# Kernel tuning notes

Hardware: AMD Instinct MI355X
Metric: run time of the kernel (lower is better)

The kernel has to match this reference:

```python
import jax, jax.numpy as jnp
import numpy as np

IMG = 1024.0            # image H = W
PRE_NMS, POST_NMS = 2000, 1000
NMS_THR, MIN_SZ = 0.7, 16.0
B = 16                  # batch of images


def _make_anchors():
    # Standard FPN anchor tiling: strides {4..64}, one scale per level, 3 ratios.
    strides = [4, 8, 16, 32, 64]
    scales = [32.0, 64.0, 128.0, 256.0, 512.0]
    ratios = [0.5, 1.0, 2.0]
    out = []
    for s, sc in zip(strides, scales):
        n = int(IMG) // s
        c = (np.arange(n, dtype=np.float32) + 0.5) * s
        xs, ys = np.meshgrid(c, c, indexing="xy")
        ctr = np.stack([xs.ravel(), ys.ravel()], -1)              # (n*n, 2) cx,cy
        wh = np.array([[sc * np.sqrt(1.0 / r), sc * np.sqrt(r)] for r in ratios],
                      dtype=np.float32)                           # (3, 2)
        b = np.concatenate([ctr[:, None, :] - wh[None] / 2,
                            ctr[:, None, :] + wh[None] / 2], -1)  # (n*n, 3, 4)
        out.append(b.reshape(-1, 4))
    return np.concatenate(out, 0).astype(np.float32)              # (261888, 4)


def setup_inputs() -> dict:
    key = jax.random.key(0)
    k1, k2 = jax.random.split(key)
    anchors = jnp.asarray(_make_anchors())
    A = anchors.shape[0]
    deltas = jax.random.normal(k1, (B, A, 4), dtype=jnp.float32) * 0.1
    scores = jax.random.uniform(k2, (B, A), dtype=jnp.float32)    # post-sigmoid objectness
    return {"anchors": anchors, "deltas": deltas, "scores": scores}


def _decode(anchors, deltas):
    # decode_boxes: deltas (tx,ty,tw,th) applied to anchors; dw/dh clamped at 4.0
    aw = anchors[:, 2] - anchors[:, 0]
    ah = anchors[:, 3] - anchors[:, 1]
    ax = anchors[:, 0] + 0.5 * aw
    ay = anchors[:, 1] + 0.5 * ah
    dx, dy = deltas[..., 0], deltas[..., 1]
    dw = jnp.minimum(deltas[..., 2], 4.0)
    dh = jnp.minimum(deltas[..., 3], 4.0)
    px = dx * aw + ax
    py = dy * ah + ay
    pw = jnp.exp(dw) * aw
    ph = jnp.exp(dh) * ah
    return jnp.stack([px - 0.5 * pw, py - 0.5 * ph,
                      px + 0.5 * pw, py + 0.5 * ph], -1)


def _box_iou(a, b):
    area_a = (a[:, 2] - a[:, 0]) * (a[:, 3] - a[:, 1])
    area_b = (b[:, 2] - b[:, 0]) * (b[:, 3] - b[:, 1])
    lt = jnp.maximum(a[:, None, :2], b[None, :, :2])
    rb = jnp.minimum(a[:, None, 2:], b[None, :, 2:])
    wh = jnp.clip(rb - lt, 0.0)
    inter = wh[..., 0] * wh[..., 1]
    return inter / (area_a[:, None] + area_b[None, :] - inter + 1e-6)


def _filter_one(props, s):
    # RegionProposalNetwork._filter: clip -> size filter -> topk(pre_nms) -> NMS -> post_nms
    x1 = jnp.clip(props[:, 0], 0.0, IMG)
    y1 = jnp.clip(props[:, 1], 0.0, IMG)
    x2 = jnp.clip(props[:, 2], 0.0, IMG)
    y2 = jnp.clip(props[:, 3], 0.0, IMG)
    valid = (x2 - x1 >= MIN_SZ) & (y2 - y1 >= MIN_SZ)
    ms = jnp.where(valid, s, -jnp.inf)                 # mask instead of boolean gather (jit)
    vals, idx = jax.lax.top_k(ms, PRE_NMS)            # sorted desc, as in scores.topk
    b = jnp.stack([x1, y1, x2, y2], -1)[idx]          # (PRE_NMS, 4)
    iou = _box_iou(b, b)                              # (PRE_NMS, PRE_NMS)
    later = jnp.arange(PRE_NMS)

    def body(i, keep):
        # suppress later boxes overlapping a still-kept box i (greedy NMS)
        sup = (iou[i] > NMS_THR) & keep[i] & (later > i)
        return keep & ~sup

    keep = jax.lax.fori_loop(0, PRE_NMS, body, jnp.ones(PRE_NMS, dtype=bool))
    fs = jnp.where(keep, vals, -jnp.inf)
    fv, fi = jax.lax.top_k(fs, POST_NMS)              # kept boxes, desc score order
    good = jnp.isfinite(fv)                           # padding mask for suppressed slots
    boxes = jnp.where(good[:, None], b[fi], 0.0)
    sc = jnp.where(good, fv, 0.0)
    return jnp.concatenate([boxes, sc[:, None]], -1)  # (POST_NMS, 5) = (x1,y1,x2,y2,score)


def reference(anchors, deltas, scores):
    props = _decode(anchors, deltas)                  # (B, A, 4)
    return jax.vmap(_filter_one)(props, scores)       # (B, POST_NMS, 5)
```

## Files before the change

kernel.cpp:

```cpp
#include <hip/hip_runtime.h>
#include <stdint.h>
#include <math.h>


#define IMGF 1024.0f
#define PRE_NMS 2000
#define POST_NMS 1000
#define NMS_THR 0.7f
#define MIN_SZ 16.0f
#define CAP 4096
#define SEL 2048
#define NW (SEL / 64)
#define CNT_STRIDE 32
#define KEY_NEGINF 0x007FFFFFu
#define MAXCHUNK 12

__device__ __forceinline__ uint32_t f2key(float f) {
  uint32_t u = __float_as_uint(f);
  return (u & 0x80000000u) ? ~u : (u | 0x80000000u);
}
__device__ __forceinline__ float key2f(uint32_t k) {
  uint32_t u = (k & 0x80000000u) ? (k & 0x7FFFFFFFu) : ~k;
  return __uint_as_float(u);
}

__device__ __forceinline__ unsigned long long readlane_u64(unsigned long long v,
                                                           int lane) {
  unsigned int lo = __builtin_amdgcn_readlane((unsigned int)v, lane);
  unsigned int hi = __builtin_amdgcn_readlane((unsigned int)(v >> 32), lane);
  return ((unsigned long long)hi << 32) | lo;
}

__device__ __forceinline__ float4 decode_clip(float4 anc, float4 dlt) {
  float aw = anc.z - anc.x;
  float ah = anc.w - anc.y;
  float ax = anc.x + 0.5f * aw;
  float ay = anc.y + 0.5f * ah;
  float dw = fminf(dlt.z, 4.0f);
  float dh = fminf(dlt.w, 4.0f);
  float px = dlt.x * aw + ax;
  float py = dlt.y * ah + ay;
  float pw = expf(dw) * aw;
  float ph = expf(dh) * ah;
  float x1 = px - 0.5f * pw, y1 = py - 0.5f * ph;
  float x2 = px + 0.5f * pw, y2 = py + 0.5f * ph;
  x1 = fminf(fmaxf(x1, 0.0f), IMGF);
  y1 = fminf(fmaxf(y1, 0.0f), IMGF);
  x2 = fminf(fmaxf(x2, 0.0f), IMGF);
  y2 = fminf(fmaxf(y2, 0.0f), IMGF);
  return make_float4(x1, y1, x2, y2);
}

__global__ void k_decode(const float4* __restrict__ anchors,
                         const float4* __restrict__ deltas,
                         const float* __restrict__ scores,
                         uint32_t* __restrict__ keys,
                         uint32_t* __restrict__ chist,
                         int A, int chunks) {
  int b = blockIdx.y;
  int t = threadIdx.x;
  int lane = t & 63;
  __shared__ uint32_t shist[256];
  shist[t] = 0;
  __syncthreads();
  int base_a = blockIdx.x * (chunks * 256);
  for (int c = 0; c < chunks; c++) {
    int a = base_a + c * 256 + t;
    bool inb = a < A;
    int ac = inb ? a : (A - 1);
    size_t i = (size_t)b * A + ac;
    float4 box = decode_clip(anchors[ac], deltas[i]);
    bool valid = (box.z - box.x >= MIN_SZ) && (box.w - box.y >= MIN_SZ);
    float ms = valid ? scores[i] : -INFINITY;
    uint32_t k = f2key(ms);
    if (inb) keys[i] = k;
    uint32_t bucket = k >> 24;
    bool fin = inb && (k != KEY_NEGINF);
    unsigned long long match = __ballot(fin);
#pragma unroll
    for (int bit = 0; bit < 8; bit++) {
      bool hb = (bucket >> bit) & 1;
      unsigned long long bb = __ballot(hb && fin);
      match &= hb ? bb : ~bb;
    }
    if (fin && (__ffsll((long long)match) - 1 == lane))
      atomicAdd(&shist[bucket], (uint32_t)__popcll(match));
  }
  __syncthreads();
  uint32_t v = shist[t];
  if (v) atomicAdd(&chist[b * 256 + t], v);
}

__global__ void k_coarse(const uint32_t* __restrict__ chist,
                         int* __restrict__ cbArr,
                         uint32_t* __restrict__ cumArr) {
  int b = blockIdx.x;
  int t = threadIdx.x;
  __shared__ uint32_t sA[256];
  sA[t] = chist[b * 256 + t];
  for (int d = 1; d < 256; d <<= 1) {
    __syncthreads();
    uint32_t v = sA[t] + ((t + d < 256) ? sA[t + d] : 0u);
    __syncthreads();
    sA[t] = v;
  }
  __syncthreads();
  if (t == 0 && sA[0] < PRE_NMS) {
    cbArr[b] = -1;
    cumArr[b] = 0;
  }
  uint32_t nxt = (t < 255) ? sA[t + 1] : 0u;
  if (sA[t] >= PRE_NMS && nxt < PRE_NMS) {
    cbArr[b] = t;
    cumArr[b] = nxt;
  }
}

__global__ void k_fine(const uint32_t* __restrict__ keys,
                       const int* __restrict__ cbArr,
                       uint32_t* __restrict__ fhist,
                       int A, int chunks) {
  int b = blockIdx.y;
  int t = threadIdx.x;
  int cb = cbArr[b];
  if (cb < 0) return;
  __shared__ uint32_t shist[256];
  shist[t] = 0;
  __syncthreads();
  int base_a = blockIdx.x * (chunks * 256);
  uint32_t cbu = (uint32_t)cb;
  for (int c = 0; c < chunks; c++) {
    int a = base_a + c * 256 + t;
    if (a >= A) break;
    uint32_t k = keys[(size_t)b * A + a];
    if ((k >> 24) == cbu && k != KEY_NEGINF)
      atomicAdd(&shist[(k >> 16) & 0xFFu], 1u);
  }
  __syncthreads();
  uint32_t v = shist[t];
  if (v) atomicAdd(&fhist[b * 256 + t], v);
}

__global__ void k_thresh(const uint32_t* __restrict__ fhist,
                         const int* __restrict__ cbArr,
                         const uint32_t* __restrict__ cumArr,
                         uint32_t* __restrict__ thresh,
                         uint32_t* __restrict__ cnts) {
  int b = blockIdx.x;
  int t = threadIdx.x;
  __shared__ uint32_t sA[256];
  if (t < 2) cnts[b * CNT_STRIDE + t] = 0;
  int cb = cbArr[b];
  if (cb < 0) {
    if (t == 0) thresh[b] = 0u;
    return;
  }
  uint32_t cumAbove = cumArr[b];
  sA[t] = fhist[b * 256 + t];
  for (int d = 1; d < 256; d <<= 1) {
    __syncthreads();
    uint32_t v = sA[t] + ((t + d < 256) ? sA[t + d] : 0u);
    __syncthreads();
    sA[t] = v;
  }
  __syncthreads();
  uint32_t nxt = (t < 255) ? sA[t + 1] : 0u;
  if (cumAbove + sA[t] >= PRE_NMS && cumAbove + nxt < PRE_NMS)
    thresh[b] = (uint32_t)((cb << 8) | t);
}

__global__ void k_gather(const uint32_t* __restrict__ keys,
                         const uint32_t* __restrict__ thresh,
                         uint32_t* __restrict__ cnts,
                         unsigned long long* __restrict__ cand_sort,
                         float4* __restrict__ sel_box,
                         float* __restrict__ sel_score,
                         int A, int chunks) {
  int b = blockIdx.y;
  int t = threadIdx.x;
  int lane = t & 63;
  int w = t >> 6;
  if (blockIdx.x < SEL / 256) {
    int r = blockIdx.x * 256 + t;
    sel_score[(size_t)b * SEL + r] = -INFINITY;
    sel_box[(size_t)b * SEL + r] = make_float4(0.0f, 0.0f, 0.0f, 0.0f);
  }
  __shared__ unsigned long long s_mA[MAXCHUNK * 4], s_mT[MAXCHUNK * 4];
  __shared__ uint32_t s_offA[MAXCHUNK * 4], s_offT[MAXCHUNK * 4];
  __shared__ uint32_t s_cA[MAXCHUNK * 4], s_cT[MAXCHUNK * 4];
  __shared__ uint32_t s_baseA, s_baseT;
  uint32_t beta = thresh[b];
  uint32_t kreg[MAXCHUNK];
  int base_a = blockIdx.x * (chunks * 256);
  for (int c = 0; c < chunks; c++) {
    int a = base_a + c * 256 + t;
    bool inb = a < A;
    uint32_t k = inb ? keys[(size_t)b * A + a] : KEY_NEGINF;
    kreg[c] = k;
    uint32_t bk = k >> 16;
    bool fin = (k != KEY_NEGINF);
    unsigned long long mA = __ballot(fin && (bk > beta));
    unsigned long long mT = __ballot(fin && (bk == beta));
    if (lane == 0) {
      s_mA[c * 4 + w] = mA;
      s_mT[c * 4 + w] = mT;
    }
  }
  __syncthreads();
  if (t < chunks * 4) {
    s_cA[t] = (uint32_t)__popcll(s_mA[t]);
    s_cT[t] = (uint32_t)__popcll(s_mT[t]);
  }
  __syncthreads();
  if (t == 0) {
    uint32_t accA = 0, accT = 0;
    for (int id = 0; id < chunks * 4; id++) {
      s_offA[id] = accA;
      accA += s_cA[id];
      s_offT[id] = accT;
      accT += s_cT[id];
    }
    s_baseA = accA ? atomicAdd(&cnts[b * CNT_STRIDE + 0], accA) : 0u;
    s_baseT = accT ? atomicAdd(&cnts[b * CNT_STRIDE + 1], accT) : 0u;
  }
  __syncthreads();
  uint32_t baseA = s_baseA, baseT = s_baseT;
  unsigned long long lower = ((unsigned long long)1 << lane) - 1;
  for (int c = 0; c < chunks; c++) {
    int id = c * 4 + w;
    unsigned long long mA = s_mA[id], mT = s_mT[id];
    bool above = (mA >> lane) & 1;
    bool tie = (mT >> lane) & 1;
    if (!(above || tie)) continue;
    int pos;
    if (above) {
      pos = (int)(baseA + s_offA[id] + (uint32_t)__popcll(mA & lower));
      if (pos >= PRE_NMS) continue;
    } else {
      pos = CAP - 1 - (int)(baseT + s_offT[id] + (uint32_t)__popcll(mT & lower));
      if (pos < PRE_NMS) continue;
    }
    int a = base_a + c * 256 + t;
    cand_sort[(size_t)b * CAP + pos] =
        ((unsigned long long)kreg[c] << 32) | (uint32_t)(~(uint32_t)a);
  }
}

__global__ void k_rank(const unsigned long long* __restrict__ cand_sort,
                       const uint32_t* __restrict__ cnts,
                       const float4* __restrict__ anchors,
                       const float4* __restrict__ deltas,
                       float4* __restrict__ sel_box,
                       float* __restrict__ sel_score, int A) {
  int b = blockIdx.y;
  int t = threadIdx.x;
  uint32_t c1 = cnts[b * CNT_STRIDE + 0];
  if (c1 > PRE_NMS) c1 = PRE_NMS;
  uint32_t c2 = cnts[b * CNT_STRIDE + 1];
  if (c2 > CAP - PRE_NMS) c2 = CAP - PRE_NMS;
  int loTie = CAP - (int)c2;
  int bs = blockIdx.x * 256;
  if (bs >= (int)c1 && bs + 256 <= loTie) return;
  int s = bs + t;
  bool live = (s < (int)c1) || (s >= loTie);
  unsigned long long myKey = live ? cand_sort[(size_t)b * CAP + s] : 0ull;
  __shared__ unsigned long long tile[256];
  int rank = 0;
  for (int ts = 0; ts < CAP; ts += 256) {
    if (ts >= (int)c1 && ts + 256 <= loTie) continue;
    int idx = ts + t;
    bool lv = (idx < (int)c1) || (idx >= loTie);
    __syncthreads();
    tile[t] = lv ? cand_sort[(size_t)b * CAP + idx] : 0ull;
    __syncthreads();
    if (live) {
#pragma unroll 8
      for (int j = 0; j < 256; j++) rank += (tile[j] > myKey) ? 1 : 0;
    }
  }
  if (live && rank < SEL) {
    uint32_t a = ~((uint32_t)myKey);
    float4 box = decode_clip(anchors[a], deltas[(size_t)b * A + a]);
    sel_score[(size_t)b * SEL + rank] = key2f((uint32_t)(myKey >> 32));
    sel_box[(size_t)b * SEL + rank] = box;
  }
}

__global__ void __launch_bounds__(64)
k_nmsmask(const float4* __restrict__ sel_box,
          unsigned long long* __restrict__ mask,
          unsigned long long* __restrict__ maskT) {
  int jb = blockIdx.x;
  int rp = blockIdx.y;
  int ib0 = rp * 4;
  if (jb < ib0) return;
  int b = blockIdx.z;
  int t = threadIdx.x;
  __shared__ float4 colb[64];
  colb[t] = sel_box[(size_t)b * SEL + jb * 64 + t];
  float4 a0 = sel_box[(size_t)b * SEL + (ib0 + 0) * 64 + t];
  float4 a1 = sel_box[(size_t)b * SEL + (ib0 + 1) * 64 + t];
  float4 a2 = sel_box[(size_t)b * SEL + (ib0 + 2) * 64 + t];
  float4 a3 = sel_box[(size_t)b * SEL + (ib0 + 3) * 64 + t];
  float ar0 = (a0.z - a0.x) * (a0.w - a0.y);
  float ar1 = (a1.z - a1.x) * (a1.w - a1.y);
  float ar2 = (a2.z - a2.x) * (a2.w - a2.y);
  float ar3 = (a3.z - a3.x) * (a3.w - a3.y);
  unsigned long long b0 = 0ull, b1 = 0ull, b2 = 0ull, b3 = 0ull;
#pragma unroll 2
  for (int jj = 0; jj < 64; jj++) {
    float4 bb = colb[jj];
    float area_b = (bb.z - bb.x) * (bb.w - bb.y);
    {
      float ltx = fmaxf(a0.x, bb.x), lty = fmaxf(a0.y, bb.y);
      float rbx = fminf(a0.z, bb.z), rby = fminf(a0.w, bb.w);
      float ww = fmaxf(rbx - ltx, 0.0f), hh = fmaxf(rby - lty, 0.0f);
      float inter = ww * hh;
      float iou = inter / (ar0 + area_b - inter + 1e-6f);
      b0 |= (iou > NMS_THR) ? (1ull << jj) : 0ull;
    }
    {
      float ltx = fmaxf(a1.x, bb.x), lty = fmaxf(a1.y, bb.y);
      float rbx = fminf(a1.z, bb.z), rby = fminf(a1.w, bb.w);
      float ww = fmaxf(rbx - ltx, 0.0f), hh = fmaxf(rby - lty, 0.0f);
      float inter = ww * hh;
      float iou = inter / (ar1 + area_b - inter + 1e-6f);
      b1 |= (iou > NMS_THR) ? (1ull << jj) : 0ull;
    }
    {
      float ltx = fmaxf(a2.x, bb.x), lty = fmaxf(a2.y, bb.y);
      float rbx = fminf(a2.z, bb.z), rby = fminf(a2.w, bb.w);
      float ww = fmaxf(rbx - ltx, 0.0f), hh = fmaxf(rby - lty, 0.0f);
      float inter = ww * hh;
      float iou = inter / (ar2 + area_b - inter + 1e-6f);
      b2 |= (iou > NMS_THR) ? (1ull << jj) : 0ull;
    }
    {
      float ltx = fmaxf(a3.x, bb.x), lty = fmaxf(a3.y, bb.y);
      float rbx = fminf(a3.z, bb.z), rby = fminf(a3.w, bb.w);
      float ww = fmaxf(rbx - ltx, 0.0f), hh = fmaxf(rby - lty, 0.0f);
      float inter = ww * hh;
      float iou = inter / (ar3 + area_b - inter + 1e-6f);
      b3 |= (iou > NMS_THR) ? (1ull << jj) : 0ull;
    }
  }
  unsigned long long diagmask = (0xFFFFFFFFFFFFFFFEull << t);
  unsigned long long bitsArr[4] = {b0, b1, b2, b3};
#pragma unroll
  for (int r = 0; r < 4; r++) {
    int ib = ib0 + r;
    if (jb < ib) continue;
    int i = ib * 64 + t;
    unsigned long long bits = bitsArr[r];
    if (jb == ib) bits &= diagmask;
    bits = (i < PRE_NMS) ? bits : 0ull;
    mask[((size_t)b * NW + jb) * SEL + i] = bits;
    if (jb == ib) {
      unsigned long long myT = 0ull;
#pragma unroll 1
      for (int jj = 0; jj < 64; jj++) {
        unsigned long long colw = __ballot((bits >> jj) & 1ull);
        if (t == jj) myT = colw;
      }
      maskT[(size_t)b * SEL + i] = myT;
    }
  }
}

__global__ void __launch_bounds__(64, 1)
k_scanout(const float4* __restrict__ sel_box,
          const float* __restrict__ sel_score,
          const unsigned long long* __restrict__ mask,
          const unsigned long long* __restrict__ maskT,
          float* __restrict__ out) {
  int b = blockIdx.x;
  int t = threadIdx.x;
  int tw = t & 31;
  __shared__ uint32_t keptList[POST_NMS + 64];
  __shared__ unsigned long long tile[2][64 * NW];
  unsigned long long removed = 0ull;
  int kc = 0;
  const unsigned long long* mb = mask + (size_t)b * NW * SEL;
  const unsigned long long* tbase = maskT + (size_t)b * SEL;
  const int lastChunk = (PRE_NMS - 1) / 64;
  int cjb = t >> 5;
  int ro = (t & 31) * 2;

  {
#pragma unroll
    for (int k = 0; k < 16; k++) {
      const unsigned long long* gp =
          mb + ((size_t)(2 * k + cjb)) * SEL + ro;
      __builtin_amdgcn_global_load_lds(
          (const __attribute__((address_space(1))) uint32_t*)gp,
          (__attribute__((address_space(3))) uint32_t*)&tile[0][k * 128],
          16, 0, 0);
    }
  }
  unsigned long long colm = tbase[t];
  uint32_t scb = __float_as_uint(sel_score[(size_t)b * SEL + t]);

  for (int chunk = 0; chunk <= lastChunk; chunk++) {
    int cur = chunk & 1;
    unsigned long long colm_n = 0ull;
    uint32_t scb_n = 0xFF800000u;
    if (chunk < lastChunk) {
#pragma unroll
      for (int k = 0; k < 16; k++) {
        const unsigned long long* gp =
            mb + ((size_t)(2 * k + cjb)) * SEL + (size_t)(chunk + 1) * 64 + ro;
        __builtin_amdgcn_global_load_lds(
            (const __attribute__((address_space(1))) uint32_t*)gp,
            (__attribute__((address_space(3))) uint32_t*)
                &tile[cur ^ 1][k * 128],
            16, 0, 0);
      }
      colm_n = tbase[(chunk + 1) * 64 + t];
      scb_n =
          __float_as_uint(sel_score[(size_t)b * SEL + (chunk + 1) * 64 + t]);
    }
    int rmax = PRE_NMS - chunk * 64;
    if (rmax > 64) rmax = 64;
    unsigned long long vb = __ballot(scb != 0xFF800000u);
    unsigned long long curw = readlane_u64(removed, chunk);
    unsigned long long range = (rmax >= 64) ? ~0ull : ((1ull << rmax) - 1ull);
    unsigned long long alive0 = ~curw & range;
    unsigned long long K = alive0;
    bool aliveb = (alive0 >> t) & 1ull;
#pragma unroll 1
    for (int it = 0; it < 64; ++it) {
      bool deadb = (colm & K) != 0ull;
      unsigned long long Kn = __ballot(aliveb && !deadb);
      if (Kn == K) break;
      K = Kn;
    }
    unsigned long long keptbits = K;
    unsigned long long kv = keptbits & vb;
    if ((kv >> t) & 1ull) {
      int rank = (int)__popcll(kv & ((1ull << t) - 1ull));
      keptList[kc + rank] = (uint32_t)(chunk * 64 + t);
    }
    kc += (int)__popcll(kv);
    if (kc >= POST_NMS) break;
    if (chunk == lastChunk) break;
    asm volatile("s_waitcnt vmcnt(18)" ::: "memory");
    __builtin_amdgcn_sched_barrier(0);
    unsigned long long acc = 0ull;
#pragma unroll
    for (int j = 0; j < 64; j++) {
      int jr = (j + tw) & 63;
      unsigned long long v = tile[cur][tw * 64 + jr];
      unsigned long long mk =
          (unsigned long long)(-(long long)((keptbits >> jr) & 1ull));
      acc |= v & mk;
    }
    unsigned long long wv = (tw >= chunk) ? ~0ull : 0ull;
    removed |= acc & wv;
    __builtin_amdgcn_sched_barrier(0);
    colm = colm_n;
    scb = scb_n;
  }
  int kcc = kc < POST_NMS ? kc : POST_NMS;
  __syncthreads();
  for (int r = t; r < POST_NMS; r += 64) {
    float4 bx = make_float4(0.0f, 0.0f, 0.0f, 0.0f);
    float sc = 0.0f;
    if (r < kcc) {
      int i = (int)keptList[r];
      bx = sel_box[(size_t)b * SEL + i];
      sc = sel_score[(size_t)b * SEL + i];
    }
    float* o = out + ((size_t)b * POST_NMS + r) * 5;
    o[0] = bx.x;
    o[1] = bx.y;
    o[2] = bx.z;
    o[3] = bx.w;
    o[4] = sc;
  }
}

extern "C" void kernel_launch(void* const* d_in, const int* in_sizes, int n_in,
                              void* d_out, int out_size, void* d_ws, size_t ws_size,
                              hipStream_t stream) {
  const float* anchors = (const float*)d_in[0];
  const float* deltas = (const float*)d_in[1];
  const float* scores = (const float*)d_in[2];
  int A = in_sizes[0] / 4;
  int BA = in_sizes[2];
  int B = BA / A;
  float* out = (float*)d_out;

  char* ws = (char*)d_ws;
  size_t off = 0;
  uint32_t* keys = (uint32_t*)(ws + off);
  off += (size_t)BA * 4;
  uint32_t* chist = (uint32_t*)(ws + off);
  off += (size_t)B * 256 * 4;
  uint32_t* fhist = (uint32_t*)(ws + off);
  off += (size_t)B * 256 * 4;
  int* cbArr = (int*)(ws + off);
  off += (size_t)B * 4;
  uint32_t* cumArr = (uint32_t*)(ws + off);
  off += (size_t)B * 4;
  uint32_t* thresh = (uint32_t*)(ws + off);
  off += (size_t)B * 4;
  off = (off + 127) & ~(size_t)127;
  uint32_t* cnts = (uint32_t*)(ws + off);
  off += (size_t)B * CNT_STRIDE * 4;
  off = (off + 15) & ~(size_t)15;
  unsigned long long* cand_sort = (unsigned long long*)(ws + off);
  off += (size_t)B * CAP * 8;
  float4* sel_box = (float4*)(ws + off);
  off += (size_t)B * SEL * 16;
  float* sel_score = (float*)(ws + off);
  off += (size_t)B * SEL * 4;
  unsigned long long* mask = (unsigned long long*)(ws + off);
  off += (size_t)B * NW * SEL * 8;
  unsigned long long* maskT = (unsigned long long*)(ws + off);
  off += (size_t)B * SEL * 8;

  int chunks = (A % (256 * 11) == 0) ? 11 : 1;
  int bpb = (A + 256 * chunks - 1) / (256 * chunks);

  hipMemsetAsync(chist, 0, (size_t)B * 256 * 4 * 2, stream);
  k_decode<<<dim3(bpb, B), 256, 0, stream>>>((const float4*)anchors,
                                             (const float4*)deltas, scores,
                                             keys, chist, A, chunks);
  k_coarse<<<B, 256, 0, stream>>>(chist, cbArr, cumArr);
  k_fine<<<dim3(bpb, B), 256, 0, stream>>>(keys, cbArr, fhist, A, chunks);
  k_thresh<<<B, 256, 0, stream>>>(fhist, cbArr, cumArr, thresh, cnts);
  k_gather<<<dim3(bpb, B), 256, 0, stream>>>(keys, thresh, cnts, cand_sort,
                                             sel_box, sel_score, A, chunks);
  k_rank<<<dim3(CAP / 256, B), 256, 0, stream>>>(cand_sort, cnts,
                                                 (const float4*)anchors,
                                                 (const float4*)deltas,
                                                 sel_box, sel_score, A);
  k_nmsmask<<<dim3(NW, 8, B), 64, 0, stream>>>(sel_box, mask, maskT);
  k_scanout<<<B, 64, 0, stream>>>(sel_box, sel_score, mask, maskT, out);
}
```

Measured before the change: 287.2 us.

## Split rank computation into parallel tile-pair counts plus scatter; replace IoU division

The single rank kernel, which looped over all key tiles per block, becomes two kernels. One computes partial rank counts for every (source tile, key tile) pair in parallel, writing them into the reused keys buffer. A second kernel sums the partials and scatters the decoded boxes. The NMS mask kernel also replaces the IoU division with a double-precision multiply-compare against the threshold, which adds FP64 work and an extra launch plus partial-count traffic.

```diff
diff --git a/kernel.cpp b/kernel.cpp
--- a/kernel.cpp
+++ b/kernel.cpp
@@ -14,6 +14,7 @@
 #define CNT_STRIDE 32
 #define KEY_NEGINF 0x007FFFFFu
 #define MAXCHUNK 12
+#define IOU_T 0x1.6666668p-1
 
 __device__ __forceinline__ uint32_t f2key(float f) {
   uint32_t u = __float_as_uint(f);
@@ -246,39 +247,68 @@
   }
 }
 
-__global__ void k_rank(const unsigned long long* __restrict__ cand_sort,
-                       const uint32_t* __restrict__ cnts,
-                       const float4* __restrict__ anchors,
-                       const float4* __restrict__ deltas,
-                       float4* __restrict__ sel_box,
-                       float* __restrict__ sel_score, int A) {
-  int b = blockIdx.y;
+__global__ void k_rankcnt(const unsigned long long* __restrict__ cand_sort,
+                          const uint32_t* __restrict__ cnts,
+                          uint32_t* __restrict__ rnk_partial) {
+  int st = blockIdx.x;
+  int kt = blockIdx.y;
+  int b = blockIdx.z;
   int t = threadIdx.x;
   uint32_t c1 = cnts[b * CNT_STRIDE + 0];
   if (c1 > PRE_NMS) c1 = PRE_NMS;
   uint32_t c2 = cnts[b * CNT_STRIDE + 1];
   if (c2 > CAP - PRE_NMS) c2 = CAP - PRE_NMS;
   int loTie = CAP - (int)c2;
-  int bs = blockIdx.x * 256;
+  int bs = st * 256, ks = kt * 256;
+  if (bs >= (int)c1 && bs + 256 <= loTie) return;
+  if (ks >= (int)c1 && ks + 256 <= loTie) return;
+  int s = bs + t;
+  bool live = (s < (int)c1) || (s >= loTie);
+  unsigned long long myKey = live ? cand_sort[(size_t)b * CAP + s] : 0ull;
+  __shared__ __attribute__((aligned(16))) unsigned long long tile[256];
+  int idx = ks + t;
+  bool lv = (idx < (int)c1) || (idx >= loTie);
+  tile[t] = lv ? cand_sort[(size_t)b * CAP + idx] : 0ull;
+  __syncthreads();
+  const ulonglong2* tile2 = (const ulonglong2*)tile;
+  int cnt = 0;
+#pragma unroll 8
+  for (int j = 0; j < 128; j++) {
+    ulonglong2 v = tile2[j];
+    cnt += (v.x > myKey) ? 1 : 0;
+    cnt += (v.y > myKey) ? 1 : 0;
+  }
+  rnk_partial[((size_t)b * 16 + kt) * CAP + s] = (uint32_t)cnt;
+}
+
+__global__ void k_scatter(const unsigned long long* __restrict__ cand_sort,
+                          const uint32_t* __restrict__ rnk_partial,
+                          const uint32_t* __restrict__ cnts,
+                          const float4* __restrict__ anchors,
+                          const float4* __restrict__ deltas,
+                          float4* __restrict__ sel_box,
+                          float* __restrict__ sel_score, int A) {
+  int st = blockIdx.x;
+  int b = blockIdx.y;
+  int t = threadIdx.x;
+  uint32_t c1 = cnts[b * CNT_STRIDE + 0];
+  if (c1 > PRE_NMS) c1 = PRE_NMS;
+  uint32_t c2 = cnts[b * CNT_STRIDE + 1];
+  if (c2 > CAP - PRE_NMS) c2 = CAP - PRE_NMS;
+  int loTie = CAP - (int)c2;
+  int bs = st * 256;
   if (bs >= (int)c1 && bs + 256 <= loTie) return;
   int s = bs + t;
   bool live = (s < (int)c1) || (s >= loTie);
-  unsigned long long myKey = live ? cand_sort[(size_t)b * CAP + s] : 0ull;
-  __shared__ unsigned long long tile[256];
+  if (!live) return;
   int rank = 0;
-  for (int ts = 0; ts < CAP; ts += 256) {
-    if (ts >= (int)c1 && ts + 256 <= loTie) continue;
-    int idx = ts + t;
-    bool lv = (idx < (int)c1) || (idx >= loTie);
-    __syncthreads();
-    tile[t] = lv ? cand_sort[(size_t)b * CAP + idx] : 0ull;
-    __syncthreads();
-    if (live) {
-#pragma unroll 8
-      for (int j = 0; j < 256; j++) rank += (tile[j] > myKey) ? 1 : 0;
-    }
-  }
-  if (live && rank < SEL) {
+  for (int kt = 0; kt < 16; kt++) {
+    int ks = kt * 256;
+    if (ks >= (int)c1 && ks + 256 <= loTie) continue;
+    rank += (int)rnk_partial[((size_t)b * 16 + kt) * CAP + s];
+  }
+  if (rank < SEL) {
+    unsigned long long myKey = cand_sort[(size_t)b * CAP + s];
     uint32_t a = ~((uint32_t)myKey);
     float4 box = decode_clip(anchors[a], deltas[(size_t)b * A + a]);
     sel_score[(size_t)b * SEL + rank] = key2f((uint32_t)(myKey >> 32));
@@ -316,32 +346,32 @@
       float rbx = fminf(a0.z, bb.z), rby = fminf(a0.w, bb.w);
       float ww = fmaxf(rbx - ltx, 0.0f), hh = fmaxf(rby - lty, 0.0f);
       float inter = ww * hh;
-      float iou = inter / (ar0 + area_b - inter + 1e-6f);
-      b0 |= (iou > NMS_THR) ? (1ull << jj) : 0ull;
+      float denom = ar0 + area_b - inter + 1e-6f;
+      b0 |= ((double)inter >= IOU_T * (double)denom) ? (1ull << jj) : 0ull;
     }
     {
       float ltx = fmaxf(a1.x, bb.x), lty = fmaxf(a1.y, bb.y);
       float rbx = fminf(a1.z, bb.z), rby = fminf(a1.w, bb.w);
       float ww = fmaxf(rbx - ltx, 0.0f), hh = fmaxf(rby - lty, 0.0f);
       float inter = ww * hh;
-      float iou = inter / (ar1 + area_b - inter + 1e-6f);
-      b1 |= (iou > NMS_THR) ? (1ull << jj) : 0ull;
+      float denom = ar1 + area_b - inter + 1e-6f;
+      b1 |= ((double)inter >= IOU_T * (double)denom) ? (1ull << jj) : 0ull;
     }
     {
       float ltx = fmaxf(a2.x, bb.x), lty = fmaxf(a2.y, bb.y);
       float rbx = fminf(a2.z, bb.z), rby = fminf(a2.w, bb.w);
       float ww = fmaxf(rbx - ltx, 0.0f), hh = fmaxf(rby - lty, 0.0f);
       float inter = ww * hh;
-      float iou = inter / (ar2 + area_b - inter + 1e-6f);
-      b2 |= (iou > NMS_THR) ? (1ull << jj) : 0ull;
+      float denom = ar2 + area_b - inter + 1e-6f;
+      b2 |= ((double)inter >= IOU_T * (double)denom) ? (1ull << jj) : 0ull;
     }
     {
       float ltx = fmaxf(a3.x, bb.x), lty = fmaxf(a3.y, bb.y);
       float rbx = fminf(a3.z, bb.z), rby = fminf(a3.w, bb.w);
       float ww = fmaxf(rbx - ltx, 0.0f), hh = fmaxf(rby - lty, 0.0f);
       float inter = ww * hh;
-      float iou = inter / (ar3 + area_b - inter + 1e-6f);
-      b3 |= (iou > NMS_THR) ? (1ull << jj) : 0ull;
+      float denom = ar3 + area_b - inter + 1e-6f;
+      b3 |= ((double)inter >= IOU_T * (double)denom) ? (1ull << jj) : 0ull;
     }
   }
   unsigned long long diagmask = (0xFFFFFFFFFFFFFFFEull << t);
@@ -518,6 +548,7 @@
   off += (size_t)B * NW * SEL * 8;
   unsigned long long* maskT = (unsigned long long*)(ws + off);
   off += (size_t)B * SEL * 8;
+  uint32_t* rnk_partial = keys;
 
   int chunks = (A % (256 * 11) == 0) ? 11 : 1;
   int bpb = (A + 256 * chunks - 1) / (256 * chunks);
@@ -531,10 +562,12 @@
   k_thresh<<<B, 256, 0, stream>>>(fhist, cbArr, cumArr, thresh, cnts);
   k_gather<<<dim3(bpb, B), 256, 0, stream>>>(keys, thresh, cnts, cand_sort,
                                              sel_box, sel_score, A, chunks);
-  k_rank<<<dim3(CAP / 256, B), 256, 0, stream>>>(cand_sort, cnts,
-                                                 (const float4*)anchors,
-                                                 (const float4*)deltas,
-                                                 sel_box, sel_score, A);
+  k_rankcnt<<<dim3(CAP / 256, CAP / 256, B), 256, 0, stream>>>(cand_sort, cnts,
+                                                               rnk_partial);
+  k_scatter<<<dim3(CAP / 256, B), 256, 0, stream>>>(cand_sort, rnk_partial,
+                                                    cnts, (const float4*)anchors,
+                                                    (const float4*)deltas,
+                                                    sel_box, sel_score, A);
   k_nmsmask<<<dim3(NW, 8, B), 64, 0, stream>>>(sel_box, mask, maskT);
   k_scanout<<<B, 64, 0, stream>>>(sel_box, sel_score, mask, maskT, out);
 }
```

Measured after the change: 250.1 us. -12.9%, faster.
